# Kernel tuning notes

Measured on AMD Instinct MI355X. Metric: run time of the kernel, lower is better.

## Reference

```python
import jax, jax.numpy as jnp
import numpy as np

B, T, M, E, H, D = 4, 1024, 1024, 1024, 16, 64
SCALE = D ** (-0.5)


def setup_inputs() -> dict:
    key = jax.random.key(0)
    ks = jax.random.split(key, 8)
    w = 0.02  # weight scale for numerical stability of softmax
    return {
        "x": jax.random.normal(ks[0], (B, T, E), jnp.float32),
        "xl_memory": jax.random.normal(ks[1], (B, M, 2, H * D), jnp.float32),
        "relative_positions": jax.random.normal(ks[2], (H, T, M + T), jnp.float32),
        "Wq": jax.random.normal(ks[3], (E, H * D), jnp.float32) * w,
        "bq": jnp.zeros((H * D,), jnp.float32),
        "Wk": jax.random.normal(ks[4], (E, H * D), jnp.float32) * w,
        "bk": jnp.zeros((H * D,), jnp.float32),
        "Wv": jax.random.normal(ks[5], (E, H * D), jnp.float32) * w,
        "bv": jnp.zeros((H * D,), jnp.float32),
        "Wo": jax.random.normal(ks[6], (H * D, E), jnp.float32) * w,
        "bo": jnp.zeros((E,), jnp.float32),
    }


def reference(x, xl_memory, relative_positions, Wq, bq, Wk, bk, Wv, bv, Wo, bo):
    b, t, _ = x.shape
    q = (x @ Wq + bq) * SCALE                     # [b, t, H*D] (scale applied to queries)
    k = x @ Wk + bk
    v = x @ Wv + bv
    k_xl = xl_memory[:, :, 0]                      # [b, m, H*D]
    v_xl = xl_memory[:, :, 1]
    m = k_xl.shape[1]
    keys = jnp.concatenate((k_xl, k), axis=1)      # [b, j, H*D], j = m + t
    values = jnp.concatenate((v_xl, v), axis=1)
    j = keys.shape[1]

    qh = q.reshape(b, t, H, D).transpose(0, 2, 1, 3)       # b h i d
    kh = keys.reshape(b, j, H, D).transpose(0, 2, 1, 3)    # b h j d
    vh = values.reshape(b, j, H, D).transpose(0, 2, 1, 3)  # b h j d

    qk = jnp.einsum("bhid,bhjd->bhij", qh, kh)
    qk = relative_positions[..., -t:, -j:] + qk
    qk = qk * SCALE                                # second scale, faithful to source
    mask = jnp.triu(jnp.ones((t, j), dtype=bool), j - t + 1)
    qk = jnp.where(mask, -jnp.inf, qk)
    attn = jax.nn.softmax(qk, axis=-1)             # dropout p=0.0 -> identity

    qkv = jnp.einsum("bhij,bhjd->bhid", attn, vh)
    qkv = qkv.transpose(0, 2, 1, 3).reshape(b, t, H * D)
    out = qkv @ Wo + bo

    kv_memories = jnp.stack((keys, values), axis=-2)  # [b, j, 2, H*D]
    kv_to_add_xl = kv_memories[:, -m:]                 # [b, m, 2, H*D]
    return out, kv_to_add_xl
```

## Files before the change

### kernel.cpp

```cpp
#include <hip/hip_runtime.h>
#include <hip/hip_bf16.h>

typedef unsigned short u16;
typedef unsigned int u32;
typedef __attribute__((ext_vector_type(8))) short short8;
typedef __attribute__((ext_vector_type(4))) float f32x4;

#define B_ 4
#define T_ 1024
#define E_ 1024
#define NH 16
#define HD 1024
#define JTOT 2048
#define SCALE 0.125f
#define LOG2E 1.44269504f

__device__ __forceinline__ u16 f2b(float f) {
  u32 x = __float_as_uint(f);
  u32 r = (x + 0x7fffu + ((x >> 16) & 1u)) >> 16;
  return (u16)r;
}
__device__ __forceinline__ u16 f2b_fast(float f) {
  return (u16)((__float_as_uint(f) + 0x8000u) >> 16);
}
__device__ __forceinline__ float fexp2(float x) {
  float r;
  asm("v_exp_f32 %0, %1" : "=v"(r) : "v"(x));
  return r;
}

__device__ __forceinline__ void gload_lds16(const void* g, void* l) {
  __builtin_amdgcn_global_load_lds((const __attribute__((address_space(1))) u32*)g,
                                   (__attribute__((address_space(3))) u32*)l, 16, 0, 0);
}

__device__ __forceinline__ short8 pack8(float4 f0, float4 f1) {
  short8 o;
  o[0] = (short)f2b(f0.x); o[1] = (short)f2b(f0.y);
  o[2] = (short)f2b(f0.z); o[3] = (short)f2b(f0.w);
  o[4] = (short)f2b(f1.x); o[5] = (short)f2b(f1.y);
  o[6] = (short)f2b(f1.z); o[7] = (short)f2b(f1.w);
  return o;
}

__global__ __launch_bounds__(256) void cvt_bf16(const float* __restrict__ in,
                                                u16* __restrict__ out, int n8) {
  int i = blockIdx.x * 256 + threadIdx.x;
  if (i >= n8) return;
  const float4* p = (const float4*)in + (size_t)i * 2;
  ((short8*)out)[i] = pack8(p[0], p[1]);
}

__global__ __launch_bounds__(256) void cvt_w4T(const float* __restrict__ Wq, const float* __restrict__ Wk,
                                               const float* __restrict__ Wv, const float* __restrict__ Wo,
                                               u16* __restrict__ wqkvT, u16* __restrict__ woT) {
  __shared__ float tile[64][65];
  const float* W;
  u16* WT;
  int z = blockIdx.z;
  if (z == 0) { W = Wq; WT = wqkvT; }
  else if (z == 1) { W = Wk; WT = wqkvT + (size_t)1024 * 1024; }
  else if (z == 2) { W = Wv; WT = wqkvT + (size_t)2048 * 1024; }
  else { W = Wo; WT = woT; }
  int t = threadIdx.x;
  int r0 = blockIdx.y * 64, c0 = blockIdx.x * 64;
#pragma unroll
  for (int i = 0; i < 16; ++i) {
    int r = i * 4 + (t >> 6), c = t & 63;
    tile[r][c] = W[(size_t)(r0 + r) * 1024 + c0 + c];
  }
  __syncthreads();
#pragma unroll
  for (int i = 0; i < 16; ++i) {
    int r = i * 4 + (t >> 6), c = t & 63;
    WT[(size_t)(c0 + r) * 1024 + r0 + c] = f2b(tile[c][r]);
  }
}

__global__ __launch_bounds__(256) void cvt_xl_k(const float* __restrict__ xl, u16* __restrict__ kt) {
  int i = blockIdx.x * 256 + threadIdx.x;
  int hd8 = i & 127, j = (i >> 7) & 1023, b = i >> 17;
  const float4* p = (const float4*)(xl + ((((size_t)b * 1024 + j) * 2 + 0) * 1024 + (size_t)hd8 * 8));
  short8 o = pack8(p[0], p[1]);
  int h = hd8 >> 3, d0 = (hd8 & 7) * 8;
  int jc = j >> 6, jl = j & 63;
  u16* dst = kt + (((size_t)(b * 16 + h) * 32 + jc) * 4096) + jl * 64 + (d0 ^ (((jl >> 2) & 3) << 4));
  *(short8*)dst = o;
}

__global__ __launch_bounds__(256) void cvt_xl_vT(const float* __restrict__ xl, u16* __restrict__ vt) {
  __shared__ u16 Vl[64 * 72];
  int bx = blockIdx.x;
  int jc = bx & 15, h = (bx >> 4) & 15, b = bx >> 8;
  int t = threadIdx.x;
  int j0 = jc * 64;
#pragma unroll
  for (int it = 0; it < 2; ++it) {
    int p = t + 256 * it;
    int j = p >> 3, d8 = p & 7;
    const float4* src = (const float4*)(xl + ((((size_t)b * 1024 + j0 + j) * 2 + 1) * 1024 + h * 64 + (size_t)d8 * 8));
    *(short8*)&Vl[j * 72 + d8 * 8] = pack8(src[0], src[1]);
  }
  __syncthreads();
#pragma unroll
  for (int it = 0; it < 2; ++it) {
    int p = t + 256 * it;
    int d = p >> 3, j8 = p & 7;
    short8 o;
#pragma unroll
    for (int e = 0; e < 8; ++e) o[e] = (short)Vl[(j8 * 8 + e) * 72 + d];
    u16* dst = vt + (((size_t)(b * 16 + h) * 32 + jc) * 4096) + d * 64 + ((j8 * 8) ^ (((d >> 2) & 3) << 4));
    *(short8*)dst = o;
  }
}

__global__ __launch_bounds__(256) void trans_vnew(const u16* __restrict__ vb, u16* __restrict__ vt) {
  __shared__ u16 Vl[64 * 72];
  int bx = blockIdx.x;
  int jcl = bx & 15, h = (bx >> 4) & 15, b = bx >> 8;
  int jc = 16 + jcl;
  int t = threadIdx.x;
  int t0 = jcl * 64;
#pragma unroll
  for (int it = 0; it < 2; ++it) {
    int p = t + 256 * it;
    int j = p >> 3, d8 = p & 7;
    *(short8*)&Vl[j * 72 + d8 * 8] =
        *(const short8*)&vb[((size_t)b * 1024 + t0 + j) * 1024 + h * 64 + d8 * 8];
  }
  __syncthreads();
#pragma unroll
  for (int it = 0; it < 2; ++it) {
    int p = t + 256 * it;
    int d = p >> 3, j8 = p & 7;
    short8 o;
#pragma unroll
    for (int e = 0; e < 8; ++e) o[e] = (short)Vl[(j8 * 8 + e) * 72 + d];
    u16* dst = vt + (((size_t)(b * 16 + h) * 32 + jc) * 4096) + d * 64 + ((j8 * 8) ^ (((d >> 2) & 3) << 4));
    *(short8*)dst = o;
  }
}

template <int MODE>
__global__ __launch_bounds__(256) void gemm128(
    const u16* __restrict__ A, const u16* __restrict__ BT,
    const float* __restrict__ b0, const float* __restrict__ b1, const float* __restrict__ b2,
    u16* __restrict__ qb, float* __restrict__ kvout, u16* __restrict__ kt, u16* __restrict__ vb,
    float* __restrict__ outf, int Ntiles, int Kdim) {
  __shared__ __align__(16) u16 As[128 * 32];
  __shared__ __align__(16) u16 Bs[128 * 32];
  const int t = threadIdx.x;
  const int lane = t & 63, wv = t >> 6;
  const int wr = wv >> 1, wc = wv & 1;
  const int m0 = (blockIdx.x / Ntiles) * 128;
  const int n0 = (blockIdx.x % Ntiles) * 128;
  const int lr = lane & 15, lg = lane >> 4;

  f32x4 acc[4][4] = {};

  for (int kc = 0; kc < Kdim; kc += 32) {
    __syncthreads();
#pragma unroll
    for (int i = 0; i < 2; ++i) {
      int p = t + 256 * i;
      gload_lds16(A + (size_t)(m0 + (p >> 2)) * Kdim + kc + (p & 3) * 8, &As[p * 8]);
    }
#pragma unroll
    for (int i = 0; i < 2; ++i) {
      int p = t + 256 * i;
      gload_lds16(BT + (size_t)(n0 + (p >> 2)) * Kdim + kc + (p & 3) * 8, &Bs[p * 8]);
    }
    __syncthreads();

    short8 af[4], bf[4];
#pragma unroll
    for (int mf = 0; mf < 4; ++mf)
      af[mf] = *(const short8*)&As[(wr * 64 + mf * 16 + lr) * 32 + lg * 8];
#pragma unroll
    for (int nf = 0; nf < 4; ++nf)
      bf[nf] = *(const short8*)&Bs[(wc * 64 + nf * 16 + lr) * 32 + lg * 8];
#pragma unroll
    for (int mf = 0; mf < 4; ++mf)
#pragma unroll
      for (int nf = 0; nf < 4; ++nf)
        acc[mf][nf] = __builtin_amdgcn_mfma_f32_16x16x32_bf16(af[mf], bf[nf], acc[mf][nf], 0, 0, 0);
  }

#pragma unroll
  for (int mf = 0; mf < 4; ++mf) {
#pragma unroll
    for (int nf = 0; nf < 4; ++nf) {
#pragma unroll
      for (int r = 0; r < 4; ++r) {
        int row = m0 + wr * 64 + mf * 16 + lg * 4 + r;
        int col = n0 + wc * 64 + nf * 16 + lr;
        float v = acc[mf][nf][r];
        if (MODE == 0) {
          int b = row >> 10, tt = row & 1023;
          if (col < 1024) {
            v += b0[col];
            qb[(size_t)row * HD + col] = f2b(v * (SCALE * SCALE * LOG2E));
          } else if (col < 2048) {
            int hd = col - 1024;
            v += b1[hd];
            kvout[((size_t)(b * 1024 + tt) * 2 + 0) * HD + hd] = v;
            int h = hd >> 6, d = hd & 63, jl = tt & 63, jc = 16 + (tt >> 6);
            kt[(((size_t)(b * 16 + h) * 32 + jc) * 4096) + jl * 64 + (d ^ (((jl >> 2) & 3) << 4))] = f2b(v);
          } else {
            int hd = col - 2048;
            v += b2[hd];
            kvout[((size_t)(b * 1024 + tt) * 2 + 1) * HD + hd] = v;
            vb[((size_t)b * 1024 + tt) * 1024 + hd] = f2b(v);
          }
        } else {
          outf[(size_t)row * E_ + col] = v + b0[col];
        }
      }
    }
  }
}

__global__ __launch_bounds__(256) void attn_kernel(
    const u16* __restrict__ qb, const u16* __restrict__ kt, const u16* __restrict__ vt,
    const float* __restrict__ rel, u16* __restrict__ aout) {
  __shared__ __align__(16) u16 Ks[2][4096];
  __shared__ __align__(16) u16 Vs[2][4096];
  __shared__ __align__(16) u16 Pl[4096];
  const int bx = blockIdx.x;
  const int b = bx & 3, h = (bx >> 2) & 15, qt = bx >> 6;
  const int i0 = qt * 64;
  const int t = threadIdx.x, lane = t & 63, w = t >> 6;
  const int lr = lane & 15, lg = lane >> 4;
  const int sel = (lr >> 2) & 3;
  const float RC = SCALE * LOG2E;

  const u16* ktb = kt + (size_t)(b * 16 + h) * 32 * 4096;
  const u16* vtb = vt + (size_t)(b * 16 + h) * 32 * 4096;
  const float* relbase = rel + (size_t)h * T_ * JTOT;
  const int ib = i0 + w * 16 + lg * 4;

  short8 qf[2];
#pragma unroll
  for (int kc = 0; kc < 2; ++kc)
    qf[kc] = *(const short8*)&qb[(size_t)(b * T_ + i0 + w * 16 + lr) * HD + h * 64 + kc * 32 + lg * 8];

  short8 vf5;
#pragma unroll
  for (int e = 0; e < 8; ++e) vf5[e] = (lr == 0) ? (short)0x3f80 : (short)0;

  const int nchunks = qt + 17;

  auto stage = [&](int buf, int jc2) {
    const u16* ksrc = ktb + (size_t)jc2 * 4096;
    const u16* vsrc = vtb + (size_t)jc2 * 4096;
    gload_lds16(ksrc + t * 8, &Ks[buf][t * 8]);
    gload_lds16(ksrc + (t + 256) * 8, &Ks[buf][(t + 256) * 8]);
    gload_lds16(vsrc + t * 8, &Vs[buf][t * 8]);
    gload_lds16(vsrc + (t + 256) * 8, &Vs[buf][(t + 256) * 8]);
  };

  float rl[4][4];
  auto loadrel = [&](int j0) {
#pragma unroll
    for (int nf = 0; nf < 4; ++nf)
#pragma unroll
      for (int r = 0; r < 4; ++r)
        rl[nf][r] = relbase[(size_t)(ib + r) * JTOT + j0 + nf * 16 + lr];
  };

  stage(0, 0);
  loadrel(0);

  f32x4 o[5] = {};
  float mrow[4];
#pragma unroll
  for (int r = 0; r < 4; ++r) mrow[r] = -__builtin_inff();

  int cur = 0;
  for (int jc = 0; jc < nchunks; ++jc) {
    __syncthreads();
    if (jc + 1 < nchunks) stage(cur ^ 1, jc + 1);

    f32x4 s4[4] = {};
#pragma unroll
    for (int nf = 0; nf < 4; ++nf)
#pragma unroll
      for (int kc = 0; kc < 2; ++kc) {
        short8 kf = *(const short8*)&Ks[cur][(nf * 16 + lr) * 64 + ((kc * 32 + lg * 8) ^ (sel << 4))];
        s4[nf] = __builtin_amdgcn_mfma_f32_16x16x32_bf16(qf[kc], kf, s4[nf], 0, 0, 0);
      }

    float p[4][4], lmax[4];
    const bool domask = (jc == qt + 16);
#pragma unroll
    for (int nf = 0; nf < 4; ++nf)
#pragma unroll
      for (int r = 0; r < 4; ++r) {
        float v = fmaf(rl[nf][r], RC, s4[nf][r]);
        if (domask && (nf * 16 + lr) > (w * 16 + lg * 4 + r)) v = -__builtin_inff();
        p[nf][r] = v;
      }
#pragma unroll
    for (int r = 0; r < 4; ++r)
      lmax[r] = fmaxf(fmaxf(p[0][r], p[1][r]), fmaxf(p[2][r], p[3][r]));
    if (jc + 1 < nchunks) loadrel((jc + 1) * 64);

    float need = -__builtin_inff();
#pragma unroll
    for (int r = 0; r < 4; ++r) need = fmaxf(need, lmax[r] - mrow[r]);
    const bool dores = !__all(need <= 11.0f);
    if (dores) {
      float chmax[4], sc[4];
#pragma unroll
      for (int r = 0; r < 4; ++r) chmax[r] = lmax[r];
#pragma unroll
      for (int msk = 1; msk <= 8; msk <<= 1)
#pragma unroll
        for (int r = 0; r < 4; ++r)
          chmax[r] = fmaxf(chmax[r], __shfl_xor(chmax[r], msk, 64));
#pragma unroll
      for (int r = 0; r < 4; ++r) {
        float nm = fmaxf(mrow[r], chmax[r]);
        sc[r] = fexp2(mrow[r] - nm);
        mrow[r] = nm;
      }
#pragma unroll
      for (int nf = 0; nf < 5; ++nf)
#pragma unroll
        for (int r = 0; r < 4; ++r) o[nf][r] *= sc[r];
    }

#pragma unroll
    for (int nf = 0; nf < 4; ++nf)
#pragma unroll
      for (int r = 0; r < 4; ++r) {
        float pe = fexp2(p[nf][r] - mrow[r]);
        Pl[(w * 16 + lg * 4 + r) * 64 + (((nf ^ lg) << 4) + lr)] = f2b_fast(pe);
      }

#pragma unroll
    for (int kc = 0; kc < 2; ++kc) {
      const int pcol = (kc * 32 + lg * 8) ^ (sel << 4);
      short8 pa = *(const short8*)&Pl[(w * 16 + lr) * 64 + pcol];
#pragma unroll
      for (int nf = 0; nf < 4; ++nf) {
        short8 vf = *(const short8*)&Vs[cur][(nf * 16 + lr) * 64 + pcol];
        o[nf] = __builtin_amdgcn_mfma_f32_16x16x32_bf16(pa, vf, o[nf], 0, 0, 0);
      }
      o[4] = __builtin_amdgcn_mfma_f32_16x16x32_bf16(pa, vf5, o[4], 0, 0, 0);
    }
    cur ^= 1;
  }

  float inv[4];
#pragma unroll
  for (int r = 0; r < 4; ++r)
    inv[r] = 1.0f / __shfl(o[4][r], lane & 48, 64);
#pragma unroll
  for (int nf = 0; nf < 4; ++nf)
#pragma unroll
    for (int r = 0; r < 4; ++r) {
      int i = i0 + w * 16 + lg * 4 + r, d = nf * 16 + lr;
      aout[(size_t)(b * T_ + i) * HD + h * 64 + d] = f2b_fast(o[nf][r] * inv[r]);
    }
}

extern "C" void kernel_launch(void* const* d_in, const int* in_sizes, int n_in,
                              void* d_out, int out_size, void* d_ws, size_t ws_size,
                              hipStream_t stream) {
  const float* x  = (const float*)d_in[0];
  const float* xl = (const float*)d_in[1];
  const float* rel = (const float*)d_in[2];
  const float* Wq = (const float*)d_in[3];
  const float* bq = (const float*)d_in[4];
  const float* Wk = (const float*)d_in[5];
  const float* bk = (const float*)d_in[6];
  const float* Wv = (const float*)d_in[7];
  const float* bv = (const float*)d_in[8];
  const float* Wo = (const float*)d_in[9];
  const float* bo = (const float*)d_in[10];

  float* out = (float*)d_out;
  float* kvout = out + (size_t)B_ * T_ * E_;

  char* ws = (char*)d_ws;
  u16* xb    = (u16*)ws; ws += (size_t)4096 * 1024 * 2;
  u16* wqkvT = (u16*)ws; ws += (size_t)3072 * 1024 * 2;
  u16* woT   = (u16*)ws; ws += (size_t)1024 * 1024 * 2;
  u16* qbuf  = (u16*)ws; ws += (size_t)4096 * 1024 * 2;
  u16* kt    = (u16*)ws; ws += (size_t)B_ * NH * 32 * 4096 * 2;
  u16* vt    = (u16*)ws; ws += (size_t)B_ * NH * 32 * 4096 * 2;
  u16* vbn   = (u16*)ws; ws += (size_t)4096 * 1024 * 2;
  u16* aout  = (u16*)ws; ws += (size_t)4096 * 1024 * 2;

  cvt_bf16<<<2048, 256, 0, stream>>>(x, xb, 524288);
  cvt_w4T<<<dim3(16, 16, 4), 256, 0, stream>>>(Wq, Wk, Wv, Wo, wqkvT, woT);
  cvt_xl_k<<<2048, 256, 0, stream>>>(xl, kt);
  cvt_xl_vT<<<1024, 256, 0, stream>>>(xl, vt);

  gemm128<0><<<32 * 24, 256, 0, stream>>>(xb, wqkvT, bq, bk, bv,
                                          qbuf, kvout, kt, vbn, nullptr, 24, 1024);
  trans_vnew<<<1024, 256, 0, stream>>>(vbn, vt);
  attn_kernel<<<1024, 256, 0, stream>>>(qbuf, kt, vt, rel, aout);
  gemm128<1><<<32 * 8, 256, 0, stream>>>(aout, woT, bo, nullptr, nullptr,
                                         nullptr, nullptr, nullptr, nullptr, out, 8, 1024);
}
```

Before: 218.6 us.

## Split attention KV range across two blocks and merge partials (split-K flash)

```diff
diff --git a/kernel.cpp b/kernel.cpp
--- a/kernel.cpp
+++ b/kernel.cpp
@@ -22,6 +22,9 @@
 }
 __device__ __forceinline__ u16 f2b_fast(float f) {
   return (u16)((__float_as_uint(f) + 0x8000u) >> 16);
+}
+__device__ __forceinline__ float b2f(u16 b) {
+  return __uint_as_float((u32)b << 16);
 }
 __device__ __forceinline__ float fexp2(float x) {
   float r;
@@ -222,18 +225,23 @@
 
 __global__ __launch_bounds__(256) void attn_kernel(
     const u16* __restrict__ qb, const u16* __restrict__ kt, const u16* __restrict__ vt,
-    const float* __restrict__ rel, u16* __restrict__ aout) {
+    const float* __restrict__ rel, u16* __restrict__ On0, u16* __restrict__ On1,
+    float* __restrict__ ml) {
   __shared__ __align__(16) u16 Ks[2][4096];
   __shared__ __align__(16) u16 Vs[2][4096];
   __shared__ __align__(16) u16 Pl[4096];
   const int bx = blockIdx.x;
-  const int b = bx & 3, h = (bx >> 2) & 15, qt = bx >> 6;
+  const int b = bx & 3, h = (bx >> 2) & 15, s = (bx >> 6) & 1, qt = bx >> 7;
   const int i0 = qt * 64;
   const int t = threadIdx.x, lane = t & 63, w = t >> 6;
   const int lr = lane & 15, lg = lane >> 4;
   const int sel = (lr >> 2) & 3;
   const float RC = SCALE * LOG2E;
 
+  const int ntot = qt + 17;
+  const int c0 = s == 0 ? 0 : (ntot + 1) >> 1;
+  const int c1 = s == 0 ? (ntot + 1) >> 1 : ntot;
+
   const u16* ktb = kt + (size_t)(b * 16 + h) * 32 * 4096;
   const u16* vtb = vt + (size_t)(b * 16 + h) * 32 * 4096;
   const float* relbase = rel + (size_t)h * T_ * JTOT;
@@ -247,8 +255,6 @@
   short8 vf5;
 #pragma unroll
   for (int e = 0; e < 8; ++e) vf5[e] = (lr == 0) ? (short)0x3f80 : (short)0;
-
-  const int nchunks = qt + 17;
 
   auto stage = [&](int buf, int jc2) {
     const u16* ksrc = ktb + (size_t)jc2 * 4096;
@@ -268,8 +274,8 @@
         rl[nf][r] = relbase[(size_t)(ib + r) * JTOT + j0 + nf * 16 + lr];
   };
 
-  stage(0, 0);
-  loadrel(0);
+  stage(0, c0);
+  loadrel(c0 * 64);
 
   f32x4 o[5] = {};
   float mrow[4];
@@ -277,11 +283,12 @@
   for (int r = 0; r < 4; ++r) mrow[r] = -__builtin_inff();
 
   int cur = 0;
-  for (int jc = 0; jc < nchunks; ++jc) {
+  for (int jc = c0; jc < c1; ++jc) {
     __syncthreads();
-    if (jc + 1 < nchunks) stage(cur ^ 1, jc + 1);
+    if (jc + 1 < c1) stage(cur ^ 1, jc + 1);
 
     f32x4 s4[4] = {};
+    __builtin_amdgcn_s_setprio(1);
 #pragma unroll
     for (int nf = 0; nf < 4; ++nf)
 #pragma unroll
@@ -289,6 +296,7 @@
         short8 kf = *(const short8*)&Ks[cur][(nf * 16 + lr) * 64 + ((kc * 32 + lg * 8) ^ (sel << 4))];
         s4[nf] = __builtin_amdgcn_mfma_f32_16x16x32_bf16(qf[kc], kf, s4[nf], 0, 0, 0);
       }
+    __builtin_amdgcn_s_setprio(0);
 
     float p[4][4], lmax[4];
     const bool domask = (jc == qt + 16);
@@ -303,7 +311,7 @@
 #pragma unroll
     for (int r = 0; r < 4; ++r)
       lmax[r] = fmaxf(fmaxf(p[0][r], p[1][r]), fmaxf(p[2][r], p[3][r]));
-    if (jc + 1 < nchunks) loadrel((jc + 1) * 64);
+    if (jc + 1 < c1) loadrel((jc + 1) * 64);
 
     float need = -__builtin_inff();
 #pragma unroll
@@ -338,6 +346,7 @@
         Pl[(w * 16 + lg * 4 + r) * 64 + (((nf ^ lg) << 4) + lr)] = f2b_fast(pe);
       }
 
+    __builtin_amdgcn_s_setprio(1);
 #pragma unroll
     for (int kc = 0; kc < 2; ++kc) {
       const int pcol = (kc * 32 + lg * 8) ^ (sel << 4);
@@ -349,20 +358,52 @@
       }
       o[4] = __builtin_amdgcn_mfma_f32_16x16x32_bf16(pa, vf5, o[4], 0, 0, 0);
     }
+    __builtin_amdgcn_s_setprio(0);
     cur ^= 1;
   }
 
-  float inv[4];
-#pragma unroll
-  for (int r = 0; r < 4; ++r)
-    inv[r] = 1.0f / __shfl(o[4][r], lane & 48, 64);
+  u16* On = (s == 0) ? On0 : On1;
+  float lsum[4], inv[4];
+#pragma unroll
+  for (int r = 0; r < 4; ++r) {
+    lsum[r] = __shfl(o[4][r], lane & 48, 64);
+    inv[r] = 1.0f / lsum[r];
+  }
 #pragma unroll
   for (int nf = 0; nf < 4; ++nf)
 #pragma unroll
     for (int r = 0; r < 4; ++r) {
-      int i = i0 + w * 16 + lg * 4 + r, d = nf * 16 + lr;
-      aout[(size_t)(b * T_ + i) * HD + h * 64 + d] = f2b_fast(o[nf][r] * inv[r]);
-    }
+      int i = ib + r, d = nf * 16 + lr;
+      On[(((size_t)(b * 16 + h) * 1024) + i) * 64 + d] = f2b_fast(o[nf][r] * inv[r]);
+    }
+  if (lr == 0) {
+#pragma unroll
+    for (int r = 0; r < 4; ++r) {
+      size_t mi = ((size_t)s * 65536 + (size_t)(b * 16 + h) * 1024 + ib + r) * 2;
+      ml[mi] = mrow[r];
+      ml[mi + 1] = lsum[r];
+    }
+  }
+}
+
+__global__ __launch_bounds__(256) void merge_kernel(
+    const u16* __restrict__ On0, const u16* __restrict__ On1,
+    const float* __restrict__ ml, u16* __restrict__ aout) {
+  int tid = blockIdx.x * 256 + threadIdx.x;
+  int d8 = tid & 7, h = (tid >> 3) & 15, i = (tid >> 7) & 1023, b = tid >> 17;
+  size_t row = (size_t)(b * 16 + h) * 1024 + i;
+  float m0 = ml[row * 2], l0 = ml[row * 2 + 1];
+  float m1 = ml[(65536 + row) * 2], l1 = ml[(65536 + row) * 2 + 1];
+  float ms = fmaxf(m0, m1);
+  float w0 = l0 * fexp2(m0 - ms), w1 = l1 * fexp2(m1 - ms);
+  float k0 = w0 / (w0 + w1), k1 = w1 / (w0 + w1);
+  short8 a = *(const short8*)&On0[row * 64 + d8 * 8];
+  short8 bvv = *(const short8*)&On1[row * 64 + d8 * 8];
+  short8 o;
+#pragma unroll
+  for (int e = 0; e < 8; ++e)
+    o[e] = (short)f2b_fast(b2f((u16)a[e]) * k0 + b2f((u16)bvv[e]) * k1);
+  *(short8*)&aout[((size_t)(b * 1024 + i)) * 1024 + h * 64 + d8 * 8] = o;
 }
 
 extern "C" void kernel_launch(void* const* d_in, const int* in_sizes, int n_in,
@@ -393,6 +434,10 @@
   u16* vbn   = (u16*)ws; ws += (size_t)4096 * 1024 * 2;
   u16* aout  = (u16*)ws; ws += (size_t)4096 * 1024 * 2;
 
+  u16* On0 = xb;
+  u16* On1 = vbn;
+  float* ml = (float*)wqkvT;
+
   cvt_bf16<<<2048, 256, 0, stream>>>(x, xb, 524288);
   cvt_w4T<<<dim3(16, 16, 4), 256, 0, stream>>>(Wq, Wk, Wv, Wo, wqkvT, woT);
   cvt_xl_k<<<2048, 256, 0, stream>>>(xl, kt);
@@ -401,7 +446,8 @@
   gemm128<0><<<32 * 24, 256, 0, stream>>>(xb, wqkvT, bq, bk, bv,
                                           qbuf, kvout, kt, vbn, nullptr, 24, 1024);
   trans_vnew<<<1024, 256, 0, stream>>>(vbn, vt);
-  attn_kernel<<<1024, 256, 0, stream>>>(qbuf, kt, vt, rel, aout);
+  attn_kernel<<<2048, 256, 0, stream>>>(qbuf, kt, vt, rel, On0, On1, ml);
+  merge_kernel<<<2048, 256, 0, stream>>>(On0, On1, ml, aout);
   gemm128<1><<<32 * 8, 256, 0, stream>>>(aout, woT, bo, nullptr, nullptr,
                                          nullptr, nullptr, nullptr, nullptr, out, 8, 1024);
 }
```

Result: slower. 228.3 us (+4.4%).
